# Kernel tuning notes

Measured on AMD Instinct MI355X. Metric: run time of the kernel, lower is better.

The kernel has to match this reference:

```python
import jax, jax.numpy as jnp
import numpy as np

N = 50000
IN_DIM, HID, OUT = 128, 64, 128
HEADS = 4
EPS_LN = 1e-5
NEG_SLOPE = 0.2


def gat_conv(x, W, a_src, a_dst, bias, src, dst, concat):
    """PyG-style GATConv. x:[N,F], W:[F,H*C], a_src/a_dst:[H,C], src/dst:[E]."""
    H, C = a_src.shape
    h = (x @ W).reshape(-1, H, C)                 # [N,H,C]
    e_src = jnp.sum(h * a_src, axis=-1)           # [N,H]
    e_dst = jnp.sum(h * a_dst, axis=-1)           # [N,H]
    e = jax.nn.leaky_relu(e_src[src] + e_dst[dst], NEG_SLOPE)  # [E,H]
    # softmax over incoming edges per destination node (numerically stable)
    m = jax.ops.segment_max(e, dst, num_segments=N)            # [N,H]
    m = jnp.where(jnp.isfinite(m), m, 0.0)
    ex = jnp.exp(e - m[dst])                                   # [E,H]
    denom = jax.ops.segment_sum(ex, dst, num_segments=N)       # [N,H]
    alpha = ex / (denom[dst] + 1e-16)                          # [E,H]
    msg = h[src] * alpha[:, :, None]                           # [E,H,C]
    out = jax.ops.segment_sum(msg, dst, num_segments=N)        # [N,H,C]
    out = out.reshape(-1, H * C) if concat else out.mean(axis=1)
    return out + bias


def layer_norm(x, gamma, beta):
    mu = jnp.mean(x, axis=-1, keepdims=True)
    var = jnp.mean(jnp.square(x - mu), axis=-1, keepdims=True)
    return (x - mu) * jax.lax.rsqrt(var + EPS_LN) * gamma + beta


def setup_inputs() -> dict:
    key = jax.random.key(0)
    ks = jax.random.split(key, 12)
    x = jax.random.normal(ks[0], (N, IN_DIM), dtype=jnp.float32)
    edge_index = jax.random.randint(ks[1], (2, 800000), 0, N, dtype=jnp.int64)
    s1 = 1.0 / np.sqrt(IN_DIM)
    W1 = jax.random.normal(ks[2], (IN_DIM, HEADS * HID), dtype=jnp.float32) * s1
    a_src1 = jax.random.normal(ks[3], (HEADS, HID), dtype=jnp.float32) * 0.1
    a_dst1 = jax.random.normal(ks[4], (HEADS, HID), dtype=jnp.float32) * 0.1
    b1 = jnp.zeros((HEADS * HID,), dtype=jnp.float32)
    s2 = 1.0 / np.sqrt(HEADS * HID)
    W2 = jax.random.normal(ks[5], (HEADS * HID, HEADS * OUT), dtype=jnp.float32) * s2
    a_src2 = jax.random.normal(ks[6], (HEADS, OUT), dtype=jnp.float32) * 0.1
    a_dst2 = jax.random.normal(ks[7], (HEADS, OUT), dtype=jnp.float32) * 0.1
    b2 = jnp.zeros((OUT,), dtype=jnp.float32)
    gamma = jnp.ones((OUT,), dtype=jnp.float32)
    beta = jnp.zeros((OUT,), dtype=jnp.float32)
    return {"x": x, "edge_index": edge_index, "W1": W1, "a_src1": a_src1,
            "a_dst1": a_dst1, "b1": b1, "W2": W2, "a_src2": a_src2,
            "a_dst2": a_dst2, "b2": b2, "gamma": gamma, "beta": beta}


def reference(x, edge_index, W1, a_src1, a_dst1, b1, W2, a_src2, a_dst2, b2, gamma, beta):
    # PyG GATConv adds self loops by default
    loop = jnp.arange(N, dtype=edge_index.dtype)
    src = jnp.concatenate([edge_index[0], loop])
    dst = jnp.concatenate([edge_index[1], loop])
    h = gat_conv(x, W1, a_src1, a_dst1, b1, src, dst, concat=True)   # [N, 256]
    h = jax.nn.relu(h)
    h = gat_conv(h, W2, a_src2, a_dst2, b2, src, dst, concat=False)  # [N, 128]
    return layer_norm(h, gamma, beta)
```

## Files before the change

### kernel.cpp

```cpp
#include <hip/hip_runtime.h>
#include <hip/hip_fp16.h>
#include <cstdint>
#include <cstddef>


constexpr int NNODES = 50000;
constexpr int NBINS = (NNODES + 255) >> 8;
constexpr int ABLOCKS = 256;

typedef unsigned short bf16_t;
typedef __attribute__((ext_vector_type(8))) short bf16x8;
typedef __attribute__((ext_vector_type(4))) float f32x4;

__device__ __forceinline__ float bf2f(bf16_t b) {
  return __uint_as_float(((unsigned int)b) << 16);
}
__device__ __forceinline__ bf16_t f2bf(float f) {
  unsigned int u = __float_as_uint(f);
  u += 0x7fffu + ((u >> 16) & 1u);
  return (bf16_t)(u >> 16);
}
__device__ __forceinline__ float4 bf4_to_f4(ushort4 v) {
  return make_float4(bf2f(v.x), bf2f(v.y), bf2f(v.z), bf2f(v.w));
}
__device__ __forceinline__ ushort4 f4_to_bf4(float4 v) {
  return make_ushort4(f2bf(v.x), f2bf(v.y), f2bf(v.z), f2bf(v.w));
}
__device__ __forceinline__ ushort f2h(float f) {
  __half h = __float2half_rn(f);
  return *(ushort*)&h;
}
__device__ __forceinline__ float h2f(ushort u) {
  __half h; *(ushort*)&h = u;
  return __half2float(h);
}
__device__ __forceinline__ float lrelu(float x) { return x > 0.f ? x : 0.2f * x; }
__device__ __forceinline__ int clampi(int v, int lo, int hi) {
  return v < lo ? lo : (v > hi ? hi : v);
}
__device__ __forceinline__ int load_edge(const void* ei, int mode, int idx) {
  if (mode) return (int)((const long long*)ei)[idx];
  return ((const int*)ei)[idx];
}


__global__ void convert_x_kernel(const float* __restrict__ x, bf16_t* __restrict__ xb,
                                 int n4) {
  int i = blockIdx.x * blockDim.x + threadIdx.x;
  if (i >= n4) return;
  float4 v = *(const float4*)(x + 4 * (size_t)i);
  *(ushort4*)(xb + 4 * (size_t)i) = f4_to_bf4(v);
}

template <int K, int NC>
__global__ void transpose_w_kernel(const float* __restrict__ W, bf16_t* __restrict__ Wt) {
  int n = blockIdx.x;
  int k = threadIdx.x;
  Wt[(size_t)n * K + k] = f2bf(W[(size_t)k * NC + n]);
}

__global__ void proj2_kernel(const float* __restrict__ W2,
                             const float* __restrict__ asrc2,
                             const float* __restrict__ adst2,
                             float* __restrict__ ws2, float* __restrict__ wd2) {
  int h = blockIdx.x;
  int k = threadIdx.x;
  const float* wrow = W2 + (size_t)k * 512 + h * 128;
  const float* as = asrc2 + h * 128;
  const float* ad = adst2 + h * 128;
  float s = 0.f, d = 0.f;
  for (int c = 0; c < 128; ++c) { s += wrow[c] * as[c]; d += wrow[c] * ad[c]; }
  ws2[h * 256 + k] = s;
  wd2[h * 256 + k] = d;
}

__global__ __launch_bounds__(1024) void wstack_kernel(const float* __restrict__ W2,
                                                      bf16_t* __restrict__ Wt2s) {
  int c = blockIdx.x;
  int t = threadIdx.x;
  int h = t >> 8, k = t & 255;
  Wt2s[(size_t)c * 1024 + t] = f2bf(W2[(size_t)k * 512 + h * 128 + c] * 0.25f);
}

__global__ void detect_kernel(const int* __restrict__ ei32, int* __restrict__ mode) {
  __shared__ int nz;
  if (threadIdx.x == 0) nz = 0;
  __syncthreads();
  int idx = 2 * threadIdx.x + 1;
  if (ei32[idx] != 0) atomicAdd(&nz, 1);
  __syncthreads();
  if (threadIdx.x == 0) mode[0] = (nz == 0) ? 1 : 0;
}

__global__ __launch_bounds__(256) void binhist_kernel(
    const void* __restrict__ ei, const int* __restrict__ modep,
    int* __restrict__ blockBin, int e0, int et, int chunk) {
  __shared__ int h[NBINS];
  int t = threadIdx.x, blk = blockIdx.x;
  for (int i = t; i < NBINS; i += 256) h[i] = 0;
  __syncthreads();
  int mode = modep[0];
  int lo = blk * chunk, hi = min(et, lo + chunk);
  for (int e = lo + t; e < hi; e += 256) {
    int dst = (e < e0) ? load_edge(ei, mode, e0 + e) : (e - e0);
    dst = clampi(dst, 0, NNODES - 1);
    atomicAdd(&h[dst >> 8], 1);
  }
  __syncthreads();
  for (int i = t; i < NBINS; i += 256) blockBin[i * ABLOCKS + blk] = h[i];
}

__global__ __launch_bounds__(ABLOCKS) void binscanA_kernel(int* __restrict__ blockBin,
                                                           int* __restrict__ binTotal) {
  __shared__ int sm[ABLOCKS];
  int b = blockIdx.x, t = threadIdx.x;
  int orig = blockBin[b * ABLOCKS + t];
  sm[t] = orig;
  __syncthreads();
  for (int off = 1; off < ABLOCKS; off <<= 1) {
    int u = (t >= off) ? sm[t - off] : 0;
    __syncthreads();
    sm[t] += u;
    __syncthreads();
  }
  blockBin[b * ABLOCKS + t] = sm[t] - orig;
  if (t == ABLOCKS - 1) binTotal[b] = sm[ABLOCKS - 1];
}

__global__ __launch_bounds__(256) void binscanB_kernel(const int* __restrict__ binTotal,
                                                       int* __restrict__ binStart) {
  __shared__ int sm[256];
  int t = threadIdx.x;
  int orig = (t < NBINS) ? binTotal[t] : 0;
  sm[t] = orig;
  __syncthreads();
  for (int off = 1; off < 256; off <<= 1) {
    int u = (t >= off) ? sm[t - off] : 0;
    __syncthreads();
    sm[t] += u;
    __syncthreads();
  }
  if (t < NBINS) binStart[t] = sm[t] - orig;
  if (t == 255) binStart[NBINS] = sm[255];
}

__global__ __launch_bounds__(256) void binscatter_kernel(
    const void* __restrict__ ei, const int* __restrict__ modep,
    const int* __restrict__ blockBin, const int* __restrict__ binStart,
    int2* __restrict__ pairs, int e0, int et, int chunk) {
  __shared__ int cur[NBINS];
  int t = threadIdx.x, blk = blockIdx.x;
  for (int i = t; i < NBINS; i += 256)
    cur[i] = binStart[i] + blockBin[i * ABLOCKS + blk];
  __syncthreads();
  int mode = modep[0];
  int lo = blk * chunk, hi = min(et, lo + chunk);
  for (int e = lo + t; e < hi; e += 256) {
    int src, dst;
    if (e < e0) { src = load_edge(ei, mode, e); dst = load_edge(ei, mode, e0 + e); }
    else        { src = dst = e - e0; }
    src = clampi(src, 0, NNODES - 1);
    dst = clampi(dst, 0, NNODES - 1);
    int p = atomicAdd(&cur[dst >> 8], 1);
    pairs[p] = make_int2(src, dst);
  }
}

__global__ __launch_bounds__(256) void csrbin_kernel(const int2* __restrict__ pairs,
                                                     const int* __restrict__ binStart,
                                                     int* __restrict__ rowptr,
                                                     int* __restrict__ col) {
  __shared__ int cnt[256];
  __shared__ int sc[256];
  int b = blockIdx.x, t = threadIdx.x;
  int node0 = b << 8;
  int es = binStart[b], ee = binStart[b + 1];
  cnt[t] = 0;
  __syncthreads();
  for (int p = es + t; p < ee; p += 256) {
    int2 pr = pairs[p];
    int d = clampi(pr.y - node0, 0, 255);
    atomicAdd(&cnt[d], 1);
  }
  __syncthreads();
  int orig = cnt[t];
  sc[t] = orig;
  __syncthreads();
  for (int off = 1; off < 256; off <<= 1) {
    int u = (t >= off) ? sc[t - off] : 0;
    __syncthreads();
    sc[t] += u;
    __syncthreads();
  }
  int excl = sc[t] - orig;
  if (node0 + t < NNODES) rowptr[node0 + t] = es + excl;
  if (b == NBINS - 1 && t == 0) rowptr[NNODES] = ee;
  cnt[t] = excl;
  __syncthreads();
  for (int p = es + t; p < ee; p += 256) {
    int2 pr = pairs[p];
    int d = clampi(pr.y - node0, 0, 255);
    int pos = atomicAdd(&cnt[d], 1);
    col[es + pos] = pr.x;
  }
}

template <int K, int NC>
__global__ __launch_bounds__(256) void gemm_mfma_kernel(const bf16_t* __restrict__ A,
                                                        const bf16_t* __restrict__ Wt,
                                                        bf16_t* __restrict__ C, int M) {
  __shared__ __align__(16) ushort As[64 * 40];
  __shared__ __align__(16) ushort Bs[64 * 40];
  const int t    = threadIdx.x;
  const int wv   = t >> 6;
  const int lane = t & 63;
  const int m    = lane & 15;
  const int quad = lane >> 4;
  const int bm = blockIdx.x * 64, bn = blockIdx.y * 64;
  const int srow = t & 63;
  const int sk8  = t >> 6;

  f32x4 acc0 = {0.f, 0.f, 0.f, 0.f};
  f32x4 acc1 = {0.f, 0.f, 0.f, 0.f};
  f32x4 acc2 = {0.f, 0.f, 0.f, 0.f};
  f32x4 acc3 = {0.f, 0.f, 0.f, 0.f};

  for (int k0 = 0; k0 < K; k0 += 32) {
    int ga = clampi(bm + srow, 0, M - 1);
    float4 av = *(const float4*)(A + (size_t)ga * K + k0 + sk8 * 8);
    *(float4*)(&As[srow * 40 + sk8 * 8]) = av;
    float4 bv = *(const float4*)(Wt + (size_t)(bn + srow) * K + k0 + sk8 * 8);
    *(float4*)(&Bs[srow * 40 + sk8 * 8]) = bv;
    __syncthreads();

    bf16x8 af = *(const bf16x8*)(&As[(wv * 16 + m) * 40 + quad * 8]);
    bf16x8 b0 = *(const bf16x8*)(&Bs[(0 * 16 + m) * 40 + quad * 8]);
    bf16x8 b1 = *(const bf16x8*)(&Bs[(1 * 16 + m) * 40 + quad * 8]);
    bf16x8 b2 = *(const bf16x8*)(&Bs[(2 * 16 + m) * 40 + quad * 8]);
    bf16x8 b3 = *(const bf16x8*)(&Bs[(3 * 16 + m) * 40 + quad * 8]);
    acc0 = __builtin_amdgcn_mfma_f32_16x16x32_bf16(af, b0, acc0, 0, 0, 0);
    acc1 = __builtin_amdgcn_mfma_f32_16x16x32_bf16(af, b1, acc1, 0, 0, 0);
    acc2 = __builtin_amdgcn_mfma_f32_16x16x32_bf16(af, b2, acc2, 0, 0, 0);
    acc3 = __builtin_amdgcn_mfma_f32_16x16x32_bf16(af, b3, acc3, 0, 0, 0);
    __syncthreads();
  }

#pragma unroll
  for (int r = 0; r < 4; ++r) {
    int row = bm + wv * 16 + quad * 4 + r;
    if (row < M) {
      size_t base = (size_t)row * NC + bn;
      C[base +  0 + m] = f2bf(acc0[r]);
      C[base + 16 + m] = f2bf(acc1[r]);
      C[base + 32 + m] = f2bf(acc2[r]);
      C[base + 48 + m] = f2bf(acc3[r]);
    }
  }
}

__global__ __launch_bounds__(256) void scores1_kernel(const bf16_t* __restrict__ h,
                                                      const float* __restrict__ asrc,
                                                      const float* __restrict__ adst,
                                                      float* __restrict__ es,
                                                      float* __restrict__ ed) {
  int node = (blockIdx.x * blockDim.x + threadIdx.x) >> 6;
  if (node >= NNODES) return;
  int lane = threadIdx.x & 63;
  float4 hv = bf4_to_f4(*(const ushort4*)(h + (size_t)node * 256 + 4 * lane));
  float4 av = *(const float4*)(asrc + 4 * lane);
  float4 dv = *(const float4*)(adst + 4 * lane);
  float ps = hv.x * av.x + hv.y * av.y + hv.z * av.z + hv.w * av.w;
  float pd = hv.x * dv.x + hv.y * dv.y + hv.z * dv.z + hv.w * dv.w;
  for (int m = 1; m < 16; m <<= 1) { ps += __shfl_xor(ps, m); pd += __shfl_xor(pd, m); }
  if ((lane & 15) == 0) {
    es[node * 4 + (lane >> 4)] = ps;
    ed[node * 4 + (lane >> 4)] = pd;
  }
}

__global__ __launch_bounds__(256) void scores2p_kernel(const bf16_t* __restrict__ out1,
                                                       const float* __restrict__ ws2,
                                                       const float* __restrict__ wd2,
                                                       float* __restrict__ es,
                                                       float* __restrict__ ed) {
  int node = (blockIdx.x * blockDim.x + threadIdx.x) >> 6;
  if (node >= NNODES) return;
  int lane = threadIdx.x & 63;
  float4 hv = bf4_to_f4(*(const ushort4*)(out1 + (size_t)node * 256 + 4 * lane));
  float4 w0 = *(const float4*)(ws2 + 0 * 256 + 4 * lane);
  float4 w1 = *(const float4*)(ws2 + 1 * 256 + 4 * lane);
  float4 w2 = *(const float4*)(ws2 + 2 * 256 + 4 * lane);
  float4 w3 = *(const float4*)(ws2 + 3 * 256 + 4 * lane);
  float4 d0 = *(const float4*)(wd2 + 0 * 256 + 4 * lane);
  float4 d1 = *(const float4*)(wd2 + 1 * 256 + 4 * lane);
  float4 d2 = *(const float4*)(wd2 + 2 * 256 + 4 * lane);
  float4 d3 = *(const float4*)(wd2 + 3 * 256 + 4 * lane);
  float s0 = hv.x * w0.x + hv.y * w0.y + hv.z * w0.z + hv.w * w0.w;
  float s1 = hv.x * w1.x + hv.y * w1.y + hv.z * w1.z + hv.w * w1.w;
  float s2 = hv.x * w2.x + hv.y * w2.y + hv.z * w2.z + hv.w * w2.w;
  float s3 = hv.x * w3.x + hv.y * w3.y + hv.z * w3.z + hv.w * w3.w;
  float t0 = hv.x * d0.x + hv.y * d0.y + hv.z * d0.z + hv.w * d0.w;
  float t1 = hv.x * d1.x + hv.y * d1.y + hv.z * d1.z + hv.w * d1.w;
  float t2 = hv.x * d2.x + hv.y * d2.y + hv.z * d2.z + hv.w * d2.w;
  float t3 = hv.x * d3.x + hv.y * d3.y + hv.z * d3.z + hv.w * d3.w;
  for (int m = 1; m < 64; m <<= 1) {
    s0 += __shfl_xor(s0, m); s1 += __shfl_xor(s1, m);
    s2 += __shfl_xor(s2, m); s3 += __shfl_xor(s3, m);
    t0 += __shfl_xor(t0, m); t1 += __shfl_xor(t1, m);
    t2 += __shfl_xor(t2, m); t3 += __shfl_xor(t3, m);
  }
  if (lane == 0) {
    es[node * 4 + 0] = s0; es[node * 4 + 1] = s1;
    es[node * 4 + 2] = s2; es[node * 4 + 3] = s3;
    ed[node * 4 + 0] = t0; ed[node * 4 + 1] = t1;
    ed[node * 4 + 2] = t2; ed[node * 4 + 3] = t3;
  }
}

__global__ __launch_bounds__(256) void alpha_kernel(
    const float* __restrict__ es, const float* __restrict__ ed,
    const int* __restrict__ rowptr, const int* __restrict__ col,
    ushort* __restrict__ alpha) {
  int node = (blockIdx.x * blockDim.x + threadIdx.x) >> 6;
  if (node >= NNODES) return;
  int lane = threadIdx.x & 63;
  int beg = rowptr[node], end = rowptr[node + 1];
  float4 edv = *(const float4*)(ed + node * 4);
  float4 l = make_float4(0.f, 0.f, 0.f, 0.f);
  for (int p = beg + lane; p < end; p += 64) {
    int s = col[p];
    float4 e = *(const float4*)(es + s * 4);
    l.x += __expf(lrelu(e.x + edv.x));
    l.y += __expf(lrelu(e.y + edv.y));
    l.z += __expf(lrelu(e.z + edv.z));
    l.w += __expf(lrelu(e.w + edv.w));
  }
  for (int off = 1; off < 64; off <<= 1) {
    l.x += __shfl_xor(l.x, off);
    l.y += __shfl_xor(l.y, off);
    l.z += __shfl_xor(l.z, off);
    l.w += __shfl_xor(l.w, off);
  }
  float4 il = make_float4(1.f / (l.x + 1e-16f), 1.f / (l.y + 1e-16f),
                          1.f / (l.z + 1e-16f), 1.f / (l.w + 1e-16f));
  for (int p = beg + lane; p < end; p += 64) {
    int s = col[p];
    float4 e = *(const float4*)(es + s * 4);
    ushort4 a;
    a.x = f2h(__expf(lrelu(e.x + edv.x)) * il.x);
    a.y = f2h(__expf(lrelu(e.y + edv.y)) * il.y);
    a.z = f2h(__expf(lrelu(e.z + edv.z)) * il.z);
    a.w = f2h(__expf(lrelu(e.w + edv.w)) * il.w);
    *(ushort4*)(alpha + (size_t)p * 4) = a;
  }
}

__global__ __launch_bounds__(256) void aggregate1_kernel(
    const bf16_t* __restrict__ h, const ushort* __restrict__ alpha,
    const int* __restrict__ rowptr, const int* __restrict__ col,
    const float* __restrict__ b1, bf16_t* __restrict__ out) {
  int node = (blockIdx.x * blockDim.x + threadIdx.x) >> 6;
  if (node >= NNODES) return;
  int lane = threadIdx.x & 63;
  int head = lane >> 4;
  int beg = rowptr[node], end = rowptr[node + 1];
  const ushort4* hb = (const ushort4*)h;
  float4 acc = make_float4(0.f, 0.f, 0.f, 0.f);
  int j = beg;
  for (; j + 4 <= end; j += 4) {
    int s0 = col[j], s1 = col[j + 1], s2 = col[j + 2], s3 = col[j + 3];
    ushort u0 = alpha[(size_t)(j + 0) * 4 + head];
    ushort u1 = alpha[(size_t)(j + 1) * 4 + head];
    ushort u2 = alpha[(size_t)(j + 2) * 4 + head];
    ushort u3 = alpha[(size_t)(j + 3) * 4 + head];
    ushort4 r0 = hb[(size_t)s0 * 64 + lane];
    ushort4 r1 = hb[(size_t)s1 * 64 + lane];
    ushort4 r2 = hb[(size_t)s2 * 64 + lane];
    ushort4 r3 = hb[(size_t)s3 * 64 + lane];
    float a0 = h2f(u0), a1 = h2f(u1), a2 = h2f(u2), a3 = h2f(u3);
    float4 v0 = bf4_to_f4(r0), v1 = bf4_to_f4(r1);
    float4 v2 = bf4_to_f4(r2), v3 = bf4_to_f4(r3);
    acc.x += a0 * v0.x + a1 * v1.x + a2 * v2.x + a3 * v3.x;
    acc.y += a0 * v0.y + a1 * v1.y + a2 * v2.y + a3 * v3.y;
    acc.z += a0 * v0.z + a1 * v1.z + a2 * v2.z + a3 * v3.z;
    acc.w += a0 * v0.w + a1 * v1.w + a2 * v2.w + a3 * v3.w;
  }
  for (; j < end; ++j) {
    int s0 = col[j];
    float a0 = h2f(alpha[(size_t)j * 4 + head]);
    float4 v0 = bf4_to_f4(hb[(size_t)s0 * 64 + lane]);
    acc.x += a0 * v0.x;
    acc.y += a0 * v0.y;
    acc.z += a0 * v0.z;
    acc.w += a0 * v0.w;
  }
  float4 bb = *(const float4*)(b1 + 4 * lane);
  float4 o;
  o.x = fmaxf(acc.x + bb.x, 0.f);
  o.y = fmaxf(acc.y + bb.y, 0.f);
  o.z = fmaxf(acc.z + bb.z, 0.f);
  o.w = fmaxf(acc.w + bb.w, 0.f);
  *(ushort4*)(out + (size_t)node * 256 + 4 * lane) = f4_to_bf4(o);
}

__device__ __forceinline__ void fma4h(float (&acc)[4][4], ushort4 q, float4 v) {
  float f0 = h2f(q.x), f1 = h2f(q.y), f2 = h2f(q.z), f3 = h2f(q.w);
  acc[0][0] += f0 * v.x; acc[0][1] += f0 * v.y; acc[0][2] += f0 * v.z; acc[0][3] += f0 * v.w;
  acc[1][0] += f1 * v.x; acc[1][1] += f1 * v.y; acc[1][2] += f1 * v.z; acc[1][3] += f1 * v.w;
  acc[2][0] += f2 * v.x; acc[2][1] += f2 * v.y; acc[2][2] += f2 * v.z; acc[2][3] += f2 * v.w;
  acc[3][0] += f3 * v.x; acc[3][1] += f3 * v.y; acc[3][2] += f3 * v.z; acc[3][3] += f3 * v.w;
}

__global__ __launch_bounds__(256) void agg2in_kernel(
    const bf16_t* __restrict__ out1, const ushort* __restrict__ alpha,
    const int* __restrict__ rowptr, const int* __restrict__ col,
    bf16_t* __restrict__ z, int n0, int n1) {
  int node = n0 + ((blockIdx.x * blockDim.x + threadIdx.x) >> 6);
  if (node >= n1) return;
  int lane = threadIdx.x & 63;
  int beg = rowptr[node], end = rowptr[node + 1];
  const ushort4* hb = (const ushort4*)out1;
  float acc[4][4] = {{0.f,0.f,0.f,0.f},{0.f,0.f,0.f,0.f},
                     {0.f,0.f,0.f,0.f},{0.f,0.f,0.f,0.f}};
  int j = beg;
  for (; j + 4 <= end; j += 4) {
    int s0 = col[j], s1 = col[j + 1], s2 = col[j + 2], s3 = col[j + 3];
    ushort4 q0 = *(const ushort4*)(alpha + (size_t)(j + 0) * 4);
    ushort4 q1 = *(const ushort4*)(alpha + (size_t)(j + 1) * 4);
    ushort4 q2 = *(const ushort4*)(alpha + (size_t)(j + 2) * 4);
    ushort4 q3 = *(const ushort4*)(alpha + (size_t)(j + 3) * 4);
    ushort4 r0 = hb[(size_t)s0 * 64 + lane];
    ushort4 r1 = hb[(size_t)s1 * 64 + lane];
    ushort4 r2 = hb[(size_t)s2 * 64 + lane];
    ushort4 r3 = hb[(size_t)s3 * 64 + lane];
    fma4h(acc, q0, bf4_to_f4(r0));
    fma4h(acc, q1, bf4_to_f4(r1));
    fma4h(acc, q2, bf4_to_f4(r2));
    fma4h(acc, q3, bf4_to_f4(r3));
  }
  for (; j < end; ++j) {
    int s0 = col[j];
    ushort4 q0 = *(const ushort4*)(alpha + (size_t)j * 4);
    ushort4 r0 = hb[(size_t)s0 * 64 + lane];
    fma4h(acc, q0, bf4_to_f4(r0));
  }
  bf16_t* zr = z + (size_t)(node - n0) * 1024 + 4 * lane;
#pragma unroll
  for (int h = 0; h < 4; ++h) {
    *(ushort4*)(zr + h * 256) =
        f4_to_bf4(make_float4(acc[h][0], acc[h][1], acc[h][2], acc[h][3]));
  }
}

__global__ __launch_bounds__(256) void gemm2ln_kernel(
    const bf16_t* __restrict__ Z, const bf16_t* __restrict__ Wt2s,
    const float* __restrict__ b2, const float* __restrict__ gamma,
    const float* __restrict__ beta, float* __restrict__ out, int n0, int M) {
  __shared__ __align__(16) ushort As[64 * 40];
  __shared__ __align__(16) ushort Bs[128 * 40];
  const int t    = threadIdx.x;
  const int wv   = t >> 6;
  const int lane = t & 63;
  const int m    = lane & 15;
  const int quad = lane >> 4;
  const int bm   = blockIdx.x * 64;

  f32x4 c0 = {0.f,0.f,0.f,0.f}, c1 = c0, c2 = c0, c3 = c0;
  f32x4 c4 = c0, c5 = c0, c6 = c0, c7 = c0;

  const int arow = t & 63, ak8 = t >> 6;
  for (int k0 = 0; k0 < 1024; k0 += 32) {
    int ga = clampi(bm + arow, 0, M - 1);
    *(float4*)(&As[arow * 40 + ak8 * 8]) =
        *(const float4*)(Z + (size_t)ga * 1024 + k0 + ak8 * 8);
    {
      int q = t;
      *(float4*)(&Bs[(q >> 2) * 40 + (q & 3) * 8]) =
          *(const float4*)(Wt2s + (size_t)(q >> 2) * 1024 + k0 + (q & 3) * 8);
      q = t + 256;
      *(float4*)(&Bs[(q >> 2) * 40 + (q & 3) * 8]) =
          *(const float4*)(Wt2s + (size_t)(q >> 2) * 1024 + k0 + (q & 3) * 8);
    }
    __syncthreads();

    bf16x8 af = *(const bf16x8*)(&As[(wv * 16 + m) * 40 + quad * 8]);
    bf16x8 b0 = *(const bf16x8*)(&Bs[(0 * 16 + m) * 40 + quad * 8]);
    bf16x8 b1 = *(const bf16x8*)(&Bs[(1 * 16 + m) * 40 + quad * 8]);
    bf16x8 b2f = *(const bf16x8*)(&Bs[(2 * 16 + m) * 40 + quad * 8]);
    bf16x8 b3 = *(const bf16x8*)(&Bs[(3 * 16 + m) * 40 + quad * 8]);
    bf16x8 b4 = *(const bf16x8*)(&Bs[(4 * 16 + m) * 40 + quad * 8]);
    bf16x8 b5 = *(const bf16x8*)(&Bs[(5 * 16 + m) * 40 + quad * 8]);
    bf16x8 b6 = *(const bf16x8*)(&Bs[(6 * 16 + m) * 40 + quad * 8]);
    bf16x8 b7 = *(const bf16x8*)(&Bs[(7 * 16 + m) * 40 + quad * 8]);
    c0 = __builtin_amdgcn_mfma_f32_16x16x32_bf16(af, b0, c0, 0, 0, 0);
    c1 = __builtin_amdgcn_mfma_f32_16x16x32_bf16(af, b1, c1, 0, 0, 0);
    c2 = __builtin_amdgcn_mfma_f32_16x16x32_bf16(af, b2f, c2, 0, 0, 0);
    c3 = __builtin_amdgcn_mfma_f32_16x16x32_bf16(af, b3, c3, 0, 0, 0);
    c4 = __builtin_amdgcn_mfma_f32_16x16x32_bf16(af, b4, c4, 0, 0, 0);
    c5 = __builtin_amdgcn_mfma_f32_16x16x32_bf16(af, b5, c5, 0, 0, 0);
    c6 = __builtin_amdgcn_mfma_f32_16x16x32_bf16(af, b6, c6, 0, 0, 0);
    c7 = __builtin_amdgcn_mfma_f32_16x16x32_bf16(af, b7, c7, 0, 0, 0);
    __syncthreads();
  }

  float b2v[8], gv[8], btv[8];
#pragma unroll
  for (int n = 0; n < 8; ++n) {
    int c = n * 16 + m;
    b2v[n] = b2[c]; gv[n] = gamma[c]; btv[n] = beta[c];
  }
#pragma unroll
  for (int r = 0; r < 4; ++r) {
    float v0 = c0[r] + b2v[0], v1 = c1[r] + b2v[1];
    float v2 = c2[r] + b2v[2], v3 = c3[r] + b2v[3];
    float v4 = c4[r] + b2v[4], v5 = c5[r] + b2v[5];
    float v6 = c6[r] + b2v[6], v7 = c7[r] + b2v[7];
    float tsum = v0 + v1 + v2 + v3 + v4 + v5 + v6 + v7;
    tsum += __shfl_xor(tsum, 1); tsum += __shfl_xor(tsum, 2);
    tsum += __shfl_xor(tsum, 4); tsum += __shfl_xor(tsum, 8);
    float mu = tsum * (1.f / 128.f);
    float d0 = v0 - mu, d1 = v1 - mu, d2 = v2 - mu, d3 = v3 - mu;
    float d4 = v4 - mu, d5 = v5 - mu, d6 = v6 - mu, d7 = v7 - mu;
    float vq = d0*d0 + d1*d1 + d2*d2 + d3*d3 + d4*d4 + d5*d5 + d6*d6 + d7*d7;
    vq += __shfl_xor(vq, 1); vq += __shfl_xor(vq, 2);
    vq += __shfl_xor(vq, 4); vq += __shfl_xor(vq, 8);
    float rinv = rsqrtf(vq * (1.f / 128.f) + 1e-5f);
    int row = bm + wv * 16 + quad * 4 + r;
    if (row < M) {
      float* orow = out + (size_t)(n0 + row) * 128;
      orow[0 * 16 + m] = d0 * rinv * gv[0] + btv[0];
      orow[1 * 16 + m] = d1 * rinv * gv[1] + btv[1];
      orow[2 * 16 + m] = d2 * rinv * gv[2] + btv[2];
      orow[3 * 16 + m] = d3 * rinv * gv[3] + btv[3];
      orow[4 * 16 + m] = d4 * rinv * gv[4] + btv[4];
      orow[5 * 16 + m] = d5 * rinv * gv[5] + btv[5];
      orow[6 * 16 + m] = d6 * rinv * gv[6] + btv[6];
      orow[7 * 16 + m] = d7 * rinv * gv[7] + btv[7];
    }
  }
}


extern "C" void kernel_launch(void* const* d_in, const int* in_sizes, int n_in,
                              void* d_out, int out_size, void* d_ws, size_t ws_size,
                              hipStream_t stream) {
  const float* x     = (const float*)d_in[0];
  const void*  ei    = d_in[1];
  const float* W1    = (const float*)d_in[2];
  const float* asrc1 = (const float*)d_in[3];
  const float* adst1 = (const float*)d_in[4];
  const float* b1    = (const float*)d_in[5];
  const float* W2    = (const float*)d_in[6];
  const float* asrc2 = (const float*)d_in[7];
  const float* adst2 = (const float*)d_in[8];
  const float* b2    = (const float*)d_in[9];
  const float* gamma = (const float*)d_in[10];
  const float* beta  = (const float*)d_in[11];
  float* out = (float*)d_out;

  const int E0 = in_sizes[1] / 2;
  const int ET = E0 + NNODES;

  char* w = (char*)d_ws;
  bf16_t* z      = (bf16_t*)(w + 0);
  int2*   pairs  = (int2*)(w + 25600000);
  bf16_t* h1     = (bf16_t*)(w + 25600000);
  bf16_t* xb     = (bf16_t*)(w + 51200000);
  bf16_t* out1   = (bf16_t*)(w + 51200000);
  ushort* alpha  = (ushort*)(w + 76800000);
  float* es    = (float*)(w + 83600000);
  float* ed    = (float*)(w + 84400000);
  bf16_t* Wt1    = (bf16_t*)(w + 85200000);
  bf16_t* Wt2s   = (bf16_t*)(w + 85300000);
  float* ws2   = (float*)(w + 85564000);
  float* wd2   = (float*)(w + 85570000);
  int* rowptr   = (int*)(w + 85600000);
  int* binStart = (int*)(w + 85800064);
  int* binTotal = (int*)(w + 85801000);
  int* blockBin = (int*)(w + 85802000);
  int* col      = (int*)(w + 86200192);
  int* mode     = (int*)(w + 89600704);

  convert_x_kernel<<<(NNODES * 128 / 4 + 255) / 256, 256, 0, stream>>>(x, xb,
                                                                       NNODES * 128 / 4);
  transpose_w_kernel<128, 256><<<256, 128, 0, stream>>>(W1, Wt1);
  proj2_kernel<<<4, 256, 0, stream>>>(W2, asrc2, adst2, ws2, wd2);
  wstack_kernel<<<128, 1024, 0, stream>>>(W2, Wt2s);

  const int CHUNK = (ET + ABLOCKS - 1) / ABLOCKS;
  detect_kernel<<<1, 256, 0, stream>>>((const int*)ei, mode);
  binhist_kernel<<<ABLOCKS, 256, 0, stream>>>(ei, mode, blockBin, E0, ET, CHUNK);
  binscanA_kernel<<<NBINS, ABLOCKS, 0, stream>>>(blockBin, binTotal);
  binscanB_kernel<<<1, 256, 0, stream>>>(binTotal, binStart);
  binscatter_kernel<<<ABLOCKS, 256, 0, stream>>>(ei, mode, blockBin, binStart, pairs,
                                                 E0, ET, CHUNK);
  csrbin_kernel<<<NBINS, 256, 0, stream>>>(pairs, binStart, rowptr, col);

  const int MB = (NNODES + 63) / 64;
  const int NODE_BLOCKS = (NNODES + 3) / 4;

  gemm_mfma_kernel<128, 256><<<dim3(MB, 4), 256, 0, stream>>>(xb, Wt1, h1, NNODES);
  scores1_kernel<<<NODE_BLOCKS, 256, 0, stream>>>(h1, asrc1, adst1, es, ed);
  alpha_kernel<<<NODE_BLOCKS, 256, 0, stream>>>(es, ed, rowptr, col, alpha);
  aggregate1_kernel<<<NODE_BLOCKS, 256, 0, stream>>>(h1, alpha, rowptr, col, b1, out1);

  scores2p_kernel<<<NODE_BLOCKS, 256, 0, stream>>>(out1, ws2, wd2, es, ed);
  alpha_kernel<<<NODE_BLOCKS, 256, 0, stream>>>(es, ed, rowptr, col, alpha);

  const int HALF = NNODES / 2;
  const int AB = (HALF * 64 + 255) / 256;
  const int GB = (HALF + 63) / 64;
  agg2in_kernel<<<AB, 256, 0, stream>>>(out1, alpha, rowptr, col, z, 0, HALF);
  gemm2ln_kernel<<<GB, 256, 0, stream>>>(z, Wt2s, b2, gamma, beta, out, 0, HALF);
  agg2in_kernel<<<AB, 256, 0, stream>>>(out1, alpha, rowptr, col, z, HALF, NNODES);
  gemm2ln_kernel<<<GB, 256, 0, stream>>>(z, Wt2s, b2, gamma, beta, out, HALF, HALF);
}
```

Baseline: 434.1 us.

## Reorder layer-1 GAT to aggregate raw inputs before per-head projection

Measured after the change: 446.5 us. 1.03x slower.

```diff
diff --git a/kernel.cpp b/kernel.cpp
--- a/kernel.cpp
+++ b/kernel.cpp
@@ -57,6 +57,21 @@
   int n = blockIdx.x;
   int k = threadIdx.x;
   Wt[(size_t)n * K + k] = f2bf(W[(size_t)k * NC + n]);
+}
+
+__global__ void proj1_kernel(const float* __restrict__ W1,
+                             const float* __restrict__ asrc1,
+                             const float* __restrict__ adst1,
+                             float* __restrict__ ws1, float* __restrict__ wd1) {
+  int h = blockIdx.x;
+  int k = threadIdx.x;
+  const float* wrow = W1 + (size_t)k * 256 + h * 64;
+  const float* as = asrc1 + h * 64;
+  const float* ad = adst1 + h * 64;
+  float s = 0.f, d = 0.f;
+  for (int c = 0; c < 64; ++c) { s += wrow[c] * as[c]; d += wrow[c] * ad[c]; }
+  ws1[h * 128 + k] = s;
+  wd1[h * 128 + k] = d;
 }
 
 __global__ void proj2_kernel(const float* __restrict__ W2,
@@ -205,76 +220,37 @@
   }
 }
 
-template <int K, int NC>
-__global__ __launch_bounds__(256) void gemm_mfma_kernel(const bf16_t* __restrict__ A,
-                                                        const bf16_t* __restrict__ Wt,
-                                                        bf16_t* __restrict__ C, int M) {
-  __shared__ __align__(16) ushort As[64 * 40];
-  __shared__ __align__(16) ushort Bs[64 * 40];
-  const int t    = threadIdx.x;
-  const int wv   = t >> 6;
-  const int lane = t & 63;
-  const int m    = lane & 15;
-  const int quad = lane >> 4;
-  const int bm = blockIdx.x * 64, bn = blockIdx.y * 64;
-  const int srow = t & 63;
-  const int sk8  = t >> 6;
-
-  f32x4 acc0 = {0.f, 0.f, 0.f, 0.f};
-  f32x4 acc1 = {0.f, 0.f, 0.f, 0.f};
-  f32x4 acc2 = {0.f, 0.f, 0.f, 0.f};
-  f32x4 acc3 = {0.f, 0.f, 0.f, 0.f};
-
-  for (int k0 = 0; k0 < K; k0 += 32) {
-    int ga = clampi(bm + srow, 0, M - 1);
-    float4 av = *(const float4*)(A + (size_t)ga * K + k0 + sk8 * 8);
-    *(float4*)(&As[srow * 40 + sk8 * 8]) = av;
-    float4 bv = *(const float4*)(Wt + (size_t)(bn + srow) * K + k0 + sk8 * 8);
-    *(float4*)(&Bs[srow * 40 + sk8 * 8]) = bv;
-    __syncthreads();
-
-    bf16x8 af = *(const bf16x8*)(&As[(wv * 16 + m) * 40 + quad * 8]);
-    bf16x8 b0 = *(const bf16x8*)(&Bs[(0 * 16 + m) * 40 + quad * 8]);
-    bf16x8 b1 = *(const bf16x8*)(&Bs[(1 * 16 + m) * 40 + quad * 8]);
-    bf16x8 b2 = *(const bf16x8*)(&Bs[(2 * 16 + m) * 40 + quad * 8]);
-    bf16x8 b3 = *(const bf16x8*)(&Bs[(3 * 16 + m) * 40 + quad * 8]);
-    acc0 = __builtin_amdgcn_mfma_f32_16x16x32_bf16(af, b0, acc0, 0, 0, 0);
-    acc1 = __builtin_amdgcn_mfma_f32_16x16x32_bf16(af, b1, acc1, 0, 0, 0);
-    acc2 = __builtin_amdgcn_mfma_f32_16x16x32_bf16(af, b2, acc2, 0, 0, 0);
-    acc3 = __builtin_amdgcn_mfma_f32_16x16x32_bf16(af, b3, acc3, 0, 0, 0);
-    __syncthreads();
-  }
-
-#pragma unroll
-  for (int r = 0; r < 4; ++r) {
-    int row = bm + wv * 16 + quad * 4 + r;
-    if (row < M) {
-      size_t base = (size_t)row * NC + bn;
-      C[base +  0 + m] = f2bf(acc0[r]);
-      C[base + 16 + m] = f2bf(acc1[r]);
-      C[base + 32 + m] = f2bf(acc2[r]);
-      C[base + 48 + m] = f2bf(acc3[r]);
-    }
-  }
-}
-
-__global__ __launch_bounds__(256) void scores1_kernel(const bf16_t* __restrict__ h,
-                                                      const float* __restrict__ asrc,
-                                                      const float* __restrict__ adst,
-                                                      float* __restrict__ es,
-                                                      float* __restrict__ ed) {
+__global__ __launch_bounds__(256) void scores1p_kernel(const bf16_t* __restrict__ xb,
+                                                       const float* __restrict__ ws1,
+                                                       const float* __restrict__ wd1,
+                                                       float* __restrict__ es,
+                                                       float* __restrict__ ed) {
   int node = (blockIdx.x * blockDim.x + threadIdx.x) >> 6;
   if (node >= NNODES) return;
   int lane = threadIdx.x & 63;
-  float4 hv = bf4_to_f4(*(const ushort4*)(h + (size_t)node * 256 + 4 * lane));
-  float4 av = *(const float4*)(asrc + 4 * lane);
-  float4 dv = *(const float4*)(adst + 4 * lane);
-  float ps = hv.x * av.x + hv.y * av.y + hv.z * av.z + hv.w * av.w;
-  float pd = hv.x * dv.x + hv.y * dv.y + hv.z * dv.z + hv.w * dv.w;
-  for (int m = 1; m < 16; m <<= 1) { ps += __shfl_xor(ps, m); pd += __shfl_xor(pd, m); }
-  if ((lane & 15) == 0) {
-    es[node * 4 + (lane >> 4)] = ps;
-    ed[node * 4 + (lane >> 4)] = pd;
+  ushort2 xv = *(const ushort2*)(xb + (size_t)node * 128 + 2 * lane);
+  float x0 = bf2f(xv.x), x1 = bf2f(xv.y);
+  float s[4], d[4];
+#pragma unroll
+  for (int h = 0; h < 4; ++h) {
+    float2 w = *(const float2*)(ws1 + h * 128 + 2 * lane);
+    float2 v = *(const float2*)(wd1 + h * 128 + 2 * lane);
+    s[h] = x0 * w.x + x1 * w.y;
+    d[h] = x0 * v.x + x1 * v.y;
+  }
+  for (int m = 1; m < 64; m <<= 1) {
+#pragma unroll
+    for (int h = 0; h < 4; ++h) {
+      s[h] += __shfl_xor(s[h], m);
+      d[h] += __shfl_xor(d[h], m);
+    }
+  }
+  if (lane == 0) {
+#pragma unroll
+    for (int h = 0; h < 4; ++h) {
+      es[node * 4 + h] = s[h];
+      ed[node * 4 + h] = d[h];
+    }
   }
 }
 
@@ -355,52 +331,117 @@
   }
 }
 
-__global__ __launch_bounds__(256) void aggregate1_kernel(
-    const bf16_t* __restrict__ h, const ushort* __restrict__ alpha,
+__global__ __launch_bounds__(256) void agg1in_kernel(
+    const bf16_t* __restrict__ xb, const ushort* __restrict__ alpha,
     const int* __restrict__ rowptr, const int* __restrict__ col,
-    const float* __restrict__ b1, bf16_t* __restrict__ out) {
+    bf16_t* __restrict__ z1) {
   int node = (blockIdx.x * blockDim.x + threadIdx.x) >> 6;
   if (node >= NNODES) return;
   int lane = threadIdx.x & 63;
-  int head = lane >> 4;
   int beg = rowptr[node], end = rowptr[node + 1];
-  const ushort4* hb = (const ushort4*)h;
-  float4 acc = make_float4(0.f, 0.f, 0.f, 0.f);
+  float acc[4][2] = {{0.f,0.f},{0.f,0.f},{0.f,0.f},{0.f,0.f}};
   int j = beg;
   for (; j + 4 <= end; j += 4) {
     int s0 = col[j], s1 = col[j + 1], s2 = col[j + 2], s3 = col[j + 3];
-    ushort u0 = alpha[(size_t)(j + 0) * 4 + head];
-    ushort u1 = alpha[(size_t)(j + 1) * 4 + head];
-    ushort u2 = alpha[(size_t)(j + 2) * 4 + head];
-    ushort u3 = alpha[(size_t)(j + 3) * 4 + head];
-    ushort4 r0 = hb[(size_t)s0 * 64 + lane];
-    ushort4 r1 = hb[(size_t)s1 * 64 + lane];
-    ushort4 r2 = hb[(size_t)s2 * 64 + lane];
-    ushort4 r3 = hb[(size_t)s3 * 64 + lane];
-    float a0 = h2f(u0), a1 = h2f(u1), a2 = h2f(u2), a3 = h2f(u3);
-    float4 v0 = bf4_to_f4(r0), v1 = bf4_to_f4(r1);
-    float4 v2 = bf4_to_f4(r2), v3 = bf4_to_f4(r3);
-    acc.x += a0 * v0.x + a1 * v1.x + a2 * v2.x + a3 * v3.x;
-    acc.y += a0 * v0.y + a1 * v1.y + a2 * v2.y + a3 * v3.y;
-    acc.z += a0 * v0.z + a1 * v1.z + a2 * v2.z + a3 * v3.z;
-    acc.w += a0 * v0.w + a1 * v1.w + a2 * v2.w + a3 * v3.w;
+    ushort4 q0 = *(const ushort4*)(alpha + (size_t)(j + 0) * 4);
+    ushort4 q1 = *(const ushort4*)(alpha + (size_t)(j + 1) * 4);
+    ushort4 q2 = *(const ushort4*)(alpha + (size_t)(j + 2) * 4);
+    ushort4 q3 = *(const ushort4*)(alpha + (size_t)(j + 3) * 4);
+    ushort2 x0 = *(const ushort2*)(xb + (size_t)s0 * 128 + 2 * lane);
+    ushort2 x1 = *(const ushort2*)(xb + (size_t)s1 * 128 + 2 * lane);
+    ushort2 x2 = *(const ushort2*)(xb + (size_t)s2 * 128 + 2 * lane);
+    ushort2 x3 = *(const ushort2*)(xb + (size_t)s3 * 128 + 2 * lane);
+    float f00 = bf2f(x0.x), f01 = bf2f(x0.y);
+    float f10 = bf2f(x1.x), f11 = bf2f(x1.y);
+    float f20 = bf2f(x2.x), f21 = bf2f(x2.y);
+    float f30 = bf2f(x3.x), f31 = bf2f(x3.y);
+#pragma unroll
+    for (int h = 0; h < 4; ++h) {
+      float a0 = h2f(((const ushort*)&q0)[h]);
+      float a1 = h2f(((const ushort*)&q1)[h]);
+      float a2 = h2f(((const ushort*)&q2)[h]);
+      float a3 = h2f(((const ushort*)&q3)[h]);
+      acc[h][0] += a0 * f00 + a1 * f10 + a2 * f20 + a3 * f30;
+      acc[h][1] += a0 * f01 + a1 * f11 + a2 * f21 + a3 * f31;
+    }
   }
   for (; j < end; ++j) {
     int s0 = col[j];
-    float a0 = h2f(alpha[(size_t)j * 4 + head]);
-    float4 v0 = bf4_to_f4(hb[(size_t)s0 * 64 + lane]);
-    acc.x += a0 * v0.x;
-    acc.y += a0 * v0.y;
-    acc.z += a0 * v0.z;
-    acc.w += a0 * v0.w;
-  }
-  float4 bb = *(const float4*)(b1 + 4 * lane);
-  float4 o;
-  o.x = fmaxf(acc.x + bb.x, 0.f);
-  o.y = fmaxf(acc.y + bb.y, 0.f);
-  o.z = fmaxf(acc.z + bb.z, 0.f);
-  o.w = fmaxf(acc.w + bb.w, 0.f);
-  *(ushort4*)(out + (size_t)node * 256 + 4 * lane) = f4_to_bf4(o);
+    ushort4 q0 = *(const ushort4*)(alpha + (size_t)j * 4);
+    ushort2 x0 = *(const ushort2*)(xb + (size_t)s0 * 128 + 2 * lane);
+    float f00 = bf2f(x0.x), f01 = bf2f(x0.y);
+#pragma unroll
+    for (int h = 0; h < 4; ++h) {
+      float a0 = h2f(((const ushort*)&q0)[h]);
+      acc[h][0] += a0 * f00;
+      acc[h][1] += a0 * f01;
+    }
+  }
+  bf16_t* zr = z1 + (size_t)node * 512 + 2 * lane;
+#pragma unroll
+  for (int h = 0; h < 4; ++h) {
+    ushort2 o;
+    o.x = f2bf(acc[h][0]);
+    o.y = f2bf(acc[h][1]);
+    *(ushort2*)(zr + h * 128) = o;
+  }
+}
+
+__global__ __launch_bounds__(256) void gemm1h_kernel(
+    const bf16_t* __restrict__ Z1, const bf16_t* __restrict__ Wt1,
+    const float* __restrict__ b1, bf16_t* __restrict__ out1, int M) {
+  __shared__ __align__(16) ushort As[64 * 40];
+  __shared__ __align__(16) ushort Bs[64 * 40];
+  const int t    = threadIdx.x;
+  const int wv   = t >> 6;
+  const int lane = t & 63;
+  const int m    = lane & 15;
+  const int quad = lane >> 4;
+  const int bm   = blockIdx.x * 64;
+  const int hd   = blockIdx.y;
+  const int srow = t & 63;
+  const int sk8  = t >> 6;
+
+  f32x4 acc0 = {0.f, 0.f, 0.f, 0.f};
+  f32x4 acc1 = {0.f, 0.f, 0.f, 0.f};
+  f32x4 acc2 = {0.f, 0.f, 0.f, 0.f};
+  f32x4 acc3 = {0.f, 0.f, 0.f, 0.f};
+
+  for (int k0 = 0; k0 < 128; k0 += 32) {
+    int ga = clampi(bm + srow, 0, M - 1);
+    *(float4*)(&As[srow * 40 + sk8 * 8]) =
+        *(const float4*)(Z1 + (size_t)ga * 512 + hd * 128 + k0 + sk8 * 8);
+    *(float4*)(&Bs[srow * 40 + sk8 * 8]) =
+        *(const float4*)(Wt1 + (size_t)(hd * 64 + srow) * 128 + k0 + sk8 * 8);
+    __syncthreads();
+
+    bf16x8 af = *(const bf16x8*)(&As[(wv * 16 + m) * 40 + quad * 8]);
+    bf16x8 b0 = *(const bf16x8*)(&Bs[(0 * 16 + m) * 40 + quad * 8]);
+    bf16x8 b1f = *(const bf16x8*)(&Bs[(1 * 16 + m) * 40 + quad * 8]);
+    bf16x8 b2 = *(const bf16x8*)(&Bs[(2 * 16 + m) * 40 + quad * 8]);
+    bf16x8 b3 = *(const bf16x8*)(&Bs[(3 * 16 + m) * 40 + quad * 8]);
+    acc0 = __builtin_amdgcn_mfma_f32_16x16x32_bf16(af, b0, acc0, 0, 0, 0);
+    acc1 = __builtin_amdgcn_mfma_f32_16x16x32_bf16(af, b1f, acc1, 0, 0, 0);
+    acc2 = __builtin_amdgcn_mfma_f32_16x16x32_bf16(af, b2, acc2, 0, 0, 0);
+    acc3 = __builtin_amdgcn_mfma_f32_16x16x32_bf16(af, b3, acc3, 0, 0, 0);
+    __syncthreads();
+  }
+
+  float bb0 = b1[hd * 64 +  0 + m];
+  float bb1 = b1[hd * 64 + 16 + m];
+  float bb2 = b1[hd * 64 + 32 + m];
+  float bb3 = b1[hd * 64 + 48 + m];
+#pragma unroll
+  for (int r = 0; r < 4; ++r) {
+    int row = bm + wv * 16 + quad * 4 + r;
+    if (row < M) {
+      size_t base = (size_t)row * 256 + hd * 64;
+      out1[base +  0 + m] = f2bf(fmaxf(acc0[r] + bb0, 0.f));
+      out1[base + 16 + m] = f2bf(fmaxf(acc1[r] + bb1, 0.f));
+      out1[base + 32 + m] = f2bf(fmaxf(acc2[r] + bb2, 0.f));
+      out1[base + 48 + m] = f2bf(fmaxf(acc3[r] + bb3, 0.f));
+    }
+  }
 }
 
 __device__ __forceinline__ void fma4h(float (&acc)[4][4], ushort4 q, float4 v) {
@@ -562,9 +603,9 @@
   const int ET = E0 + NNODES;
 
   char* w = (char*)d_ws;
+  int2*   pairs  = (int2*)(w + 0);
+  bf16_t* z1     = (bf16_t*)(w + 0);
   bf16_t* z      = (bf16_t*)(w + 0);
-  int2*   pairs  = (int2*)(w + 25600000);
-  bf16_t* h1     = (bf16_t*)(w + 25600000);
   bf16_t* xb     = (bf16_t*)(w + 51200000);
   bf16_t* out1   = (bf16_t*)(w + 51200000);
   ushort* alpha  = (ushort*)(w + 76800000);
@@ -574,6 +615,8 @@
   bf16_t* Wt2s   = (bf16_t*)(w + 85300000);
   float* ws2   = (float*)(w + 85564000);
   float* wd2   = (float*)(w + 85570000);
+  float* ws1   = (float*)(w + 85576000);
+  float* wd1   = (float*)(w + 85580000);
   int* rowptr   = (int*)(w + 85600000);
   int* binStart = (int*)(w + 85800064);
   int* binTotal = (int*)(w + 85801000);
@@ -584,6 +627,7 @@
   convert_x_kernel<<<(NNODES * 128 / 4 + 255) / 256, 256, 0, stream>>>(x, xb,
                                                                        NNODES * 128 / 4);
   transpose_w_kernel<128, 256><<<256, 128, 0, stream>>>(W1, Wt1);
+  proj1_kernel<<<4, 128, 0, stream>>>(W1, asrc1, adst1, ws1, wd1);
   proj2_kernel<<<4, 256, 0, stream>>>(W2, asrc2, adst2, ws2, wd2);
   wstack_kernel<<<128, 1024, 0, stream>>>(W2, Wt2s);
 
@@ -599,10 +643,10 @@
   const int MB = (NNODES + 63) / 64;
   const int NODE_BLOCKS = (NNODES + 3) / 4;
 
-  gemm_mfma_kernel<128, 256><<<dim3(MB, 4), 256, 0, stream>>>(xb, Wt1, h1, NNODES);
-  scores1_kernel<<<NODE_BLOCKS, 256, 0, stream>>>(h1, asrc1, adst1, es, ed);
+  scores1p_kernel<<<NODE_BLOCKS, 256, 0, stream>>>(xb, ws1, wd1, es, ed);
   alpha_kernel<<<NODE_BLOCKS, 256, 0, stream>>>(es, ed, rowptr, col, alpha);
-  aggregate1_kernel<<<NODE_BLOCKS, 256, 0, stream>>>(h1, alpha, rowptr, col, b1, out1);
+  agg1in_kernel<<<NODE_BLOCKS, 256, 0, stream>>>(xb, alpha, rowptr, col, z1);
+  gemm1h_kernel<<<dim3(MB, 4), 256, 0, stream>>>(z1, Wt1, b1, out1, NNODES);
 
   scores2p_kernel<<<NODE_BLOCKS, 256, 0, stream>>>(out1, ws2, wd2, es, ed);
   alpha_kernel<<<NODE_BLOCKS, 256, 0, stream>>>(es, ed, rowptr, col, alpha);
```
